# Kernel tuning notes

Hardware: AMD Instinct MI355X
Metric: run time of the kernel (lower is better)

Reference implementation:

```python
import jax, jax.numpy as jnp
import numpy as np

N_NODES = 200000
N_EDGES = 600000
NODE_IN = 32
EDGE_IN = 16
HID = 128
L = 3
MLP_HID = 128
LN_EPS = 1e-5


def _dense(k, fan_in, fan_out):
    kw, kb = jax.random.split(k)
    s = 1.0 / np.sqrt(fan_in)
    W = jax.random.uniform(kw, (fan_in, fan_out), jnp.float32, -s, s)
    b = jax.random.uniform(kb, (fan_out,), jnp.float32, -s, s)
    return W, b


def setup_inputs() -> dict:
    key = jax.random.key(0)
    ks = jax.random.split(key, 16)
    x = jax.random.normal(ks[0], (N_NODES, NODE_IN), jnp.float32)
    edge_index = jax.random.randint(ks[1], (2, N_EDGES), 0, N_NODES, jnp.int32)
    edge_attr = jax.random.normal(ks[2], (N_EDGES, EDGE_IN), jnp.float32)
    enc_w, enc_b = _dense(ks[3], NODE_IN, HID)
    ee_w, ee_b = _dense(ks[4], EDGE_IN, HID)
    w1s, b1s, w2s, b2s = [], [], [], []
    for i in range(L):
        W1, B1 = _dense(jax.random.fold_in(ks[5], i), HID, HID)
        W2, B2 = _dense(jax.random.fold_in(ks[6], i), HID, HID)
        w1s.append(W1); b1s.append(B1); w2s.append(W2); b2s.append(B2)
    gine_w1 = jnp.stack(w1s); gine_b1 = jnp.stack(b1s)
    gine_w2 = jnp.stack(w2s); gine_b2 = jnp.stack(b2s)
    gine_eps = jnp.zeros((L,), jnp.float32)  # PyG GINEConv default eps=0
    ln_g = jnp.ones((L, HID), jnp.float32)
    ln_b = jnp.zeros((L, HID), jnp.float32)
    mlp_w1, mlp_b1 = _dense(ks[7], 3 * HID, MLP_HID)
    mlp_w2, mlp_b2 = _dense(ks[8], MLP_HID, 1)
    return {"x": x, "edge_index": edge_index, "edge_attr": edge_attr,
            "enc_w": enc_w, "enc_b": enc_b, "ee_w": ee_w, "ee_b": ee_b,
            "gine_w1": gine_w1, "gine_b1": gine_b1, "gine_w2": gine_w2,
            "gine_b2": gine_b2, "gine_eps": gine_eps, "ln_g": ln_g, "ln_b": ln_b,
            "mlp_w1": mlp_w1, "mlp_b1": mlp_b1, "mlp_w2": mlp_w2, "mlp_b2": mlp_b2}


def reference(x, edge_index, edge_attr, enc_w, enc_b, ee_w, ee_b,
              gine_w1, gine_b1, gine_w2, gine_b2, gine_eps, ln_g, ln_b,
              mlp_w1, mlp_b1, mlp_w2, mlp_b2):
    src, dst = edge_index[0], edge_index[1]
    h = x @ enc_w + enc_b                      # [N, HID]
    e = edge_attr @ ee_w + ee_b                # [E, HID]
    for i in range(L):
        # GINEConv: out = MLP((1+eps)*x + sum_{j->i} relu(x_j + e_ji))
        msg = jax.nn.relu(h[src] + e)          # [E, HID] gather+fuse
        agg = jax.ops.segment_sum(msg, dst, num_segments=N_NODES)
        z = (1.0 + gine_eps[i]) * h + agg
        z = jax.nn.relu(z @ gine_w1[i] + gine_b1[i]) @ gine_w2[i] + gine_b2[i]
        # PyG LayerNorm (default mode='graph'): normalize over all nodes+features
        mu = jnp.mean(z)
        zc = z - mu
        var = jnp.mean(zc * zc)
        z = zc / jnp.sqrt(var + LN_EPS) * ln_g[i] + ln_b[i]
        h = jax.nn.relu(z)                     # dropout is identity at inference
    edge_inputs = jnp.concatenate([h[src], h[dst], e], axis=1)  # [E, 3*HID]
    hmid = jax.nn.relu(edge_inputs @ mlp_w1 + mlp_b1)
    logits = (hmid @ mlp_w2 + mlp_b2)[:, 0]    # [E]
    return logits
```

## Files before the change

### kernel.cpp

```cpp
#include <hip/hip_runtime.h>
#include <hip/hip_bf16.h>

#define N_NODES 200000
#define N_EDGES 600000
#define NODE_IN 32
#define EDGE_IN 16
#define HID     128
#define LN_EPS  1e-5f
#define SCAN_B  512
#define NBLK_SCAN 391

typedef __attribute__((ext_vector_type(8))) short short8;
typedef __attribute__((ext_vector_type(4))) float f32x4;

static __device__ __forceinline__ ushort f2b(float f) {
    unsigned u = __builtin_bit_cast(unsigned, f);
    unsigned r = (u + 0x7fffu + ((u >> 16) & 1u)) >> 16;
    return (ushort)r;
}
static __device__ __forceinline__ float b2f(ushort us) {
    unsigned u = ((unsigned)us) << 16;
    return __builtin_bit_cast(float, u);
}

__global__ __launch_bounds__(256) void k_csr_zero(int* __restrict__ deg)
{
    const int i = blockIdx.x * 256 + threadIdx.x;
    if (i < N_NODES) deg[i] = 0;
}

__global__ __launch_bounds__(256) void k_csr_deg(
    const int* __restrict__ ei, int* __restrict__ deg)
{
    const int e = blockIdx.x * 256 + threadIdx.x;
    if (e < N_EDGES) atomicAdd(&deg[ei[N_EDGES + e]], 1);
}

__global__ __launch_bounds__(SCAN_B) void k_scan1(
    const int* __restrict__ deg, int* __restrict__ part)
{
    __shared__ int s[SCAN_B];
    const int t = threadIdx.x, i = blockIdx.x * SCAN_B + t;
    s[t] = (i < N_NODES) ? deg[i] : 0;
    __syncthreads();
    for (int off = SCAN_B / 2; off; off >>= 1) {
        if (t < off) s[t] += s[t + off];
        __syncthreads();
    }
    if (t == 0) part[blockIdx.x] = s[0];
}

__global__ void k_scan2(int* __restrict__ part, int* __restrict__ rowptr)
{
    if (threadIdx.x == 0) {
        int run = 0;
        for (int b = 0; b < NBLK_SCAN; b++) { int x = part[b]; part[b] = run; run += x; }
        rowptr[N_NODES] = N_EDGES;
    }
}

__global__ __launch_bounds__(SCAN_B) void k_scan3(
    const int* __restrict__ deg, const int* __restrict__ part,
    int* __restrict__ rowptr, int* __restrict__ cursor)
{
    __shared__ int s[SCAN_B];
    const int t = threadIdx.x, i = blockIdx.x * SCAN_B + t;
    const int v = (i < N_NODES) ? deg[i] : 0;
    s[t] = v;
    __syncthreads();
    for (int off = 1; off < SCAN_B; off <<= 1) {
        int x = (t >= off) ? s[t - off] : 0;
        __syncthreads();
        s[t] += x;
        __syncthreads();
    }
    if (i < N_NODES) {
        const int ex = s[t] - v + part[blockIdx.x];
        rowptr[i] = ex;
        cursor[i] = ex;
    }
}

__global__ __launch_bounds__(256) void k_csr_fill(
    const int* __restrict__ ei, const float* __restrict__ ea,
    int* __restrict__ cursor, int* __restrict__ srcp,
    int* __restrict__ dstp, float* __restrict__ eap)
{
    const int e = blockIdx.x * 256 + threadIdx.x;
    if (e < N_EDGES) {
        const int d = ei[N_EDGES + e];
        const int slot = atomicAdd(&cursor[d], 1);
        srcp[slot] = ei[e];
        dstp[slot] = d;
        const float4* s4 = (const float4*)(ea + (size_t)e * EDGE_IN);
        float4* o4 = (float4*)(eap + (size_t)slot * EDGE_IN);
        o4[0] = s4[0]; o4[1] = s4[1]; o4[2] = s4[2]; o4[3] = s4[3];
    }
}

__global__ __launch_bounds__(256) void k_prep_g(
    const float* __restrict__ gw1, const float* __restrict__ gw2,
    ushort* __restrict__ wpk)
{
    const int gidx = blockIdx.x * 256 + threadIdx.x;
    const int m    = gidx >> 11;
    const int r    = gidx & 2047;
    const int lane = r & 63;
    const int ntkb = r >> 6;
    const int nt = ntkb & 7, kb = ntkb >> 3;
    const int n  = nt * 16 + (lane & 15);
    const int k0 = kb * 32 + (lane >> 4) * 8;
    const float* W = (m < 3) ? gw1 + (size_t)m * HID * HID
                             : gw2 + (size_t)(m - 3) * HID * HID;
    short8 v;
#pragma unroll
    for (int j = 0; j < 8; j++)
        v[j] = (short)f2b(W[(size_t)(k0 + j) * HID + n]);
    ((short8*)wpk)[gidx] = v;
}

__global__ __launch_bounds__(256) void k_prep_m(
    const float* __restrict__ mw1, ushort* __restrict__ w1p)
{
    const int gidx = blockIdx.x * 256 + threadIdx.x;
    const int lane = gidx & 63;
    const int ntkb = gidx >> 6;
    const int nt = ntkb & 7, kb = ntkb >> 3;
    const int n  = nt * 16 + (lane & 15);
    const int k0 = kb * 32 + (lane >> 4) * 8;
    short8 v;
#pragma unroll
    for (int j = 0; j < 8; j++)
        v[j] = (short)f2b(mw1[(size_t)(k0 + j) * HID + n]);
    ((short8*)w1p)[gidx] = v;
}

__global__ __launch_bounds__(256) void k_node_enc(
    const float* __restrict__ x, const float* __restrict__ w,
    const float* __restrict__ b, const float* __restrict__ epsp,
    ushort* __restrict__ hz, float* __restrict__ agg,
    float* __restrict__ red)
{
    __shared__ float sx[16][NODE_IN];
    const int tid = threadIdx.x;
    const int n0  = blockIdx.x * 16;
    float* sxf = &sx[0][0];
    sxf[tid]       = x[(size_t)n0 * NODE_IN + tid];
    sxf[tid + 256] = x[(size_t)n0 * NODE_IN + tid + 256];

    const int f   = tid & 127;
    const int grp = tid >> 7;
    float wcol[NODE_IN];
#pragma unroll
    for (int k = 0; k < NODE_IN; k++) wcol[k] = w[k * HID + f];
    const float bf = b[f];
    const float alpha = 1.0f + epsp[0];
    __syncthreads();

#pragma unroll
    for (int it = 0; it < 8; it++) {
        const int ln = it * 2 + grp;
        const int n  = n0 + ln;
        const float4* sx4 = (const float4*)sx[ln];
        float acc = bf;
#pragma unroll
        for (int k4 = 0; k4 < NODE_IN / 4; k4++) {
            float4 v = sx4[k4];
            acc += v.x * wcol[k4*4] + v.y * wcol[k4*4+1] +
                   v.z * wcol[k4*4+2] + v.w * wcol[k4*4+3];
        }
        hz[(size_t)n * HID + f]  = f2b(acc);
        agg[(size_t)n * HID + f] = alpha * acc;
    }
    if (blockIdx.x == 0 && tid == 0) { red[0] = 0.f; red[1] = 0.f; }
}

__global__ __launch_bounds__(256) void k_msg2(
    const ushort* __restrict__ hz, const int* __restrict__ srcp,
    const int* __restrict__ dstp, const float* __restrict__ eap,
    const float* __restrict__ eew, const float* __restrict__ eeb,
    float* __restrict__ agg)
{
    const int tid = threadIdx.x;
    const int f   = tid & 127;
    const int s0  = blockIdx.x * 16 + (tid >> 7) * 8;

    float wcol[EDGE_IN];
#pragma unroll
    for (int k = 0; k < EDGE_IN; k++) wcol[k] = eew[k * HID + f];
    const float bf = eeb[f];

    int   prev = dstp[s0];
    float sum  = 0.f;
#pragma unroll
    for (int it = 0; it < 8; it++) {
        const int s  = s0 + it;
        const int d  = dstp[s];
        const int sn = srcp[s];
        const float4* e4 = (const float4*)(eap + (size_t)s * EDGE_IN);
        float4 a0 = e4[0], a1 = e4[1], a2 = e4[2], a3 = e4[3];
        float ev = bf;
        ev += a0.x*wcol[0]  + a0.y*wcol[1]  + a0.z*wcol[2]  + a0.w*wcol[3];
        ev += a1.x*wcol[4]  + a1.y*wcol[5]  + a1.z*wcol[6]  + a1.w*wcol[7];
        ev += a2.x*wcol[8]  + a2.y*wcol[9]  + a2.z*wcol[10] + a2.w*wcol[11];
        ev += a3.x*wcol[12] + a3.y*wcol[13] + a3.z*wcol[14] + a3.w*wcol[15];
        const float m = fmaxf(b2f(hz[(size_t)sn * HID + f]) + ev, 0.f);
        if (d != prev) {
            atomicAdd(&agg[(size_t)prev * HID + f], sum);
            prev = d; sum = m;
        } else {
            sum += m;
        }
    }
    atomicAdd(&agg[(size_t)prev * HID + f], sum);
}

template<bool IN_BF16, bool RELU_OUT, bool REDUCE>
__global__ __launch_bounds__(256) void k_gemm(
    const void* in_, const short8* __restrict__ wp,
    const float* __restrict__ bias, ushort* out, float* __restrict__ red)
{
    __shared__ ushort sU[64][136];
    const int tid = threadIdx.x;
    const int m0  = blockIdx.x * 64;

    if constexpr (IN_BF16) {
        const short8* in8 = (const short8*)((const ushort*)in_ + (size_t)m0 * HID);
#pragma unroll
        for (int it = 0; it < 4; it++) {
            const int q = it * 256 + tid;
            const int r = q >> 4, c8 = q & 15;
            *(short8*)&sU[r][c8 * 8] = in8[q];
        }
    } else {
        const float4* in4 = (const float4*)((const float*)in_ + (size_t)m0 * HID);
#pragma unroll
        for (int it = 0; it < 8; it++) {
            const int q = it * 256 + tid;
            const int r = q >> 5, c4 = q & 31;
            float4 v = in4[q];
            ushort4 u;
            u.x = f2b(v.x); u.y = f2b(v.y); u.z = f2b(v.z); u.w = f2b(v.w);
            *(ushort4*)&sU[r][c4 * 4] = u;
        }
    }
    __syncthreads();

    const int lane = tid & 63;
    const int r0   = (tid >> 6) * 16;
    const int arow = r0 + (lane & 15);
    const int kg8  = (lane >> 4) * 8;
    f32x4 acc[8] = {};
    for (int kb = 0; kb < 4; kb++) {
        short8 af = *(const short8*)&sU[arow][kb * 32 + kg8];
#pragma unroll
        for (int nt = 0; nt < 8; nt++) {
            short8 bf8 = wp[(kb * 8 + nt) * 64 + lane];
            acc[nt] = __builtin_amdgcn_mfma_f32_16x16x32_bf16(af, bf8, acc[nt], 0, 0, 0);
        }
    }

    float lsum = 0.f, lsq = 0.f;
    const int rowb = m0 + r0 + (lane >> 4) * 4;
#pragma unroll
    for (int nt = 0; nt < 8; nt++) {
        const int c = nt * 16 + (lane & 15);
        const float bc = bias[c];
#pragma unroll
        for (int j = 0; j < 4; j++) {
            float o = acc[nt][j] + bc;
            if constexpr (RELU_OUT) o = fmaxf(o, 0.f);
            if constexpr (REDUCE) { lsum += o; lsq += o * o; }
            out[(size_t)(rowb + j) * HID + c] = f2b(o);
        }
    }

    if constexpr (REDUCE) {
#pragma unroll
        for (int off = 32; off; off >>= 1) {
            lsum += __shfl_down(lsum, off);
            lsq  += __shfl_down(lsq, off);
        }
        __shared__ float sws[4], swq[4];
        const int wid = tid >> 6;
        if ((tid & 63) == 0) { sws[wid] = lsum; swq[wid] = lsq; }
        __syncthreads();
        if (tid == 0) {
            atomicAdd(&red[0], sws[0] + sws[1] + sws[2] + sws[3]);
            atomicAdd(&red[1], swq[0] + swq[1] + swq[2] + swq[3]);
        }
    }
}

__global__ void k_lnfin(float* __restrict__ red)
{
    if (threadIdx.x == 0) {
        const float inv = 1.0f / ((float)N_NODES * (float)HID);
        const float mu  = red[0] * inv;
        const float var = red[1] * inv - mu * mu;
        red[2] = mu;
        red[3] = 1.0f / sqrtf(var + LN_EPS);
        red[0] = 0.f; red[1] = 0.f;
    }
}

template<bool FUSE_NEXT>
__global__ __launch_bounds__(256) void k_ln(
    ushort* hz, const float* __restrict__ red,
    const float* __restrict__ g, const float* __restrict__ b,
    const float* __restrict__ eps_next, float* __restrict__ agg)
{
    const float mu = red[2], rstd = red[3];
    const int i = blockIdx.x * 256 + threadIdx.x;
    short8 z8 = ((const short8*)hz)[i];
    const int cb = (i & 15) * 2;
    float4 g0 = ((const float4*)g)[cb],  g1 = ((const float4*)g)[cb + 1];
    float4 b0 = ((const float4*)b)[cb],  b1 = ((const float4*)b)[cb + 1];
    float o[8];
    o[0] = fmaxf((b2f((ushort)z8[0]) - mu) * rstd * g0.x + b0.x, 0.f);
    o[1] = fmaxf((b2f((ushort)z8[1]) - mu) * rstd * g0.y + b0.y, 0.f);
    o[2] = fmaxf((b2f((ushort)z8[2]) - mu) * rstd * g0.z + b0.z, 0.f);
    o[3] = fmaxf((b2f((ushort)z8[3]) - mu) * rstd * g0.w + b0.w, 0.f);
    o[4] = fmaxf((b2f((ushort)z8[4]) - mu) * rstd * g1.x + b1.x, 0.f);
    o[5] = fmaxf((b2f((ushort)z8[5]) - mu) * rstd * g1.y + b1.y, 0.f);
    o[6] = fmaxf((b2f((ushort)z8[6]) - mu) * rstd * g1.z + b1.z, 0.f);
    o[7] = fmaxf((b2f((ushort)z8[7]) - mu) * rstd * g1.w + b1.w, 0.f);
    short8 h8;
#pragma unroll
    for (int j = 0; j < 8; j++) h8[j] = (short)f2b(o[j]);
    ((short8*)hz)[i] = h8;
    if constexpr (FUSE_NEXT) {
        const float a = 1.0f + eps_next[0];
        float4 A0, A1;
        A0.x = a*o[0]; A0.y = a*o[1]; A0.z = a*o[2]; A0.w = a*o[3];
        A1.x = a*o[4]; A1.y = a*o[5]; A1.z = a*o[6]; A1.w = a*o[7];
        ((float4*)agg)[i * 2]     = A0;
        ((float4*)agg)[i * 2 + 1] = A1;
    }
}

__global__ __launch_bounds__(256) void k_mlp(
    const ushort* __restrict__ hz, const int* __restrict__ ei,
    const float* __restrict__ ea, const float* __restrict__ eew,
    const float* __restrict__ eeb,
    const ushort* __restrict__ w1p, const float* __restrict__ b1,
    const float* __restrict__ w2, const float* __restrict__ b2,
    float* __restrict__ out)
{
    __shared__ ushort sE[64][136];
    const int* __restrict__ src = ei;
    const int* __restrict__ dst = ei + N_EDGES;
    const int tid = threadIdx.x;
    const int e0  = blockIdx.x * 64;
    const int lane = tid & 63;
    const int wv   = tid >> 6;
    const int r0   = wv * 16;

    {
        const int f = tid & 127;
        float wcol[EDGE_IN];
#pragma unroll
        for (int k = 0; k < EDGE_IN; k++) wcol[k] = eew[k * HID + f];
        const float bf = eeb[f];
#pragma unroll
        for (int it = 0; it < 32; it++) {
            const int e = it * 2 + (tid >> 7);
            const float4* ea4 = (const float4*)(ea + (size_t)(e0 + e) * EDGE_IN);
            float ev = bf;
#pragma unroll
            for (int k4 = 0; k4 < EDGE_IN / 4; k4++) {
                float4 v = ea4[k4];
                ev += v.x * wcol[k4*4] + v.y * wcol[k4*4+1] +
                      v.z * wcol[k4*4+2] + v.w * wcol[k4*4+3];
            }
            sE[e][f] = f2b(ev);
        }
    }

    const int er = e0 + r0 + (lane & 15);
    const int kg = lane >> 4;
    const int ns = src[er], nd = dst[er];
    const short8* hb8 = (const short8*)hz;
    short8 af[8];
#pragma unroll
    for (int kb = 0; kb < 4; kb++) af[kb]     = hb8[(size_t)ns * 16 + kb * 4 + kg];
#pragma unroll
    for (int kb = 0; kb < 4; kb++) af[4 + kb] = hb8[(size_t)nd * 16 + kb * 4 + kg];
    __syncthreads();

    f32x4 acc[8] = {};
    const short8* bfr = (const short8*)w1p;
#pragma unroll
    for (int kb = 0; kb < 8; kb++) {
#pragma unroll
        for (int nt = 0; nt < 8; nt++) {
            short8 bfrag = bfr[(kb * 8 + nt) * 64 + lane];
            acc[nt] = __builtin_amdgcn_mfma_f32_16x16x32_bf16(af[kb], bfrag, acc[nt], 0, 0, 0);
        }
    }
#pragma unroll
    for (int kb = 8; kb < 12; kb++) {
        short8 ae = *(const short8*)&sE[r0 + (lane & 15)][(kb - 8) * 32 + kg * 8];
#pragma unroll
        for (int nt = 0; nt < 8; nt++) {
            short8 bfrag = bfr[(kb * 8 + nt) * 64 + lane];
            acc[nt] = __builtin_amdgcn_mfma_f32_16x16x32_bf16(ae, bfrag, acc[nt], 0, 0, 0);
        }
    }

    float s0 = 0.f, s1 = 0.f, s2 = 0.f, s3 = 0.f;
#pragma unroll
    for (int nt = 0; nt < 8; nt++) {
        const int col = nt * 16 + (lane & 15);
        const float b1c = b1[col];
        const float w2c = w2[col];
        s0 += fmaxf(acc[nt][0] + b1c, 0.f) * w2c;
        s1 += fmaxf(acc[nt][1] + b1c, 0.f) * w2c;
        s2 += fmaxf(acc[nt][2] + b1c, 0.f) * w2c;
        s3 += fmaxf(acc[nt][3] + b1c, 0.f) * w2c;
    }
#pragma unroll
    for (int m = 1; m < 16; m <<= 1) {
        s0 += __shfl_xor(s0, m); s1 += __shfl_xor(s1, m);
        s2 += __shfl_xor(s2, m); s3 += __shfl_xor(s3, m);
    }
    if ((lane & 15) == 0) {
        const float bb = b2[0];
        const int eb = e0 + r0 + kg * 4;
        out[eb + 0] = s0 + bb; out[eb + 1] = s1 + bb;
        out[eb + 2] = s2 + bb; out[eb + 3] = s3 + bb;
    }
}

extern "C" void kernel_launch(void* const* d_in, const int* in_sizes, int n_in,
                              void* d_out, int out_size, void* d_ws, size_t ws_size,
                              hipStream_t stream)
{
    const float* x    = (const float*)d_in[0];
    const int*   ei   = (const int*)  d_in[1];
    const float* ea   = (const float*)d_in[2];
    const float* encw = (const float*)d_in[3];
    const float* encb = (const float*)d_in[4];
    const float* eew  = (const float*)d_in[5];
    const float* eeb  = (const float*)d_in[6];
    const float* gw1  = (const float*)d_in[7];
    const float* gb1  = (const float*)d_in[8];
    const float* gw2  = (const float*)d_in[9];
    const float* gb2  = (const float*)d_in[10];
    const float* geps = (const float*)d_in[11];
    const float* lng  = (const float*)d_in[12];
    const float* lnb  = (const float*)d_in[13];
    const float* mw1  = (const float*)d_in[14];
    const float* mb1  = (const float*)d_in[15];
    const float* mw2  = (const float*)d_in[16];
    const float* mb2  = (const float*)d_in[17];

    float* ws = (float*)d_ws;
    const size_t NH = (size_t)N_NODES * HID;
    float*  agg  = ws;
    ushort* hz   = (ushort*)(ws + NH);
    float*  eap  = ws + NH + NH / 2;
    int*    srcp = (int*)(ws + 48000000);
    int*    dstp = (int*)(ws + 48600000);
    int*    deg  = (int*)(ws + 49200000);
    int*    rowp = (int*)(ws + 49400000);
    int*    curs = (int*)(ws + 49600064);
    int*    part = (int*)(ws + 49800064);
    float*  red  = ws + 49800640;
    ushort* wpk  = (ushort*)(ws + 49800704);
    ushort* w1p  = (ushort*)(ws + 49850000);

    k_prep_g<<<48, 256, 0, stream>>>(gw1, gw2, wpk);
    k_prep_m<<<24, 256, 0, stream>>>(mw1, w1p);
    k_csr_zero<<<(N_NODES + 255) / 256, 256, 0, stream>>>(deg);
    k_csr_deg<<<(N_EDGES + 255) / 256, 256, 0, stream>>>(ei, deg);
    k_scan1<<<NBLK_SCAN, SCAN_B, 0, stream>>>(deg, part);
    k_scan2<<<1, 64, 0, stream>>>(part, rowp);
    k_scan3<<<NBLK_SCAN, SCAN_B, 0, stream>>>(deg, part, rowp, curs);
    k_csr_fill<<<(N_EDGES + 255) / 256, 256, 0, stream>>>(ei, ea, curs,
                                                          srcp, dstp, eap);
    k_node_enc<<<N_NODES / 16, 256, 0, stream>>>(x, encw, encb, geps, hz, agg, red);

    const int LN_BLKS = (int)(NH / 8 / 256);
    for (int l = 0; l < 3; l++) {
        k_msg2<<<N_EDGES / 16, 256, 0, stream>>>(hz, srcp, dstp, eap,
                                                 eew, eeb, agg);
        k_gemm<false, true, false><<<N_NODES / 64, 256, 0, stream>>>(
            agg, (const short8*)wpk + (size_t)l * 2048,
            gb1 + (size_t)l * HID, hz, nullptr);
        k_gemm<true, false, true><<<N_NODES / 64, 256, 0, stream>>>(
            hz, (const short8*)wpk + (size_t)(3 + l) * 2048,
            gb2 + (size_t)l * HID, hz, red);
        k_lnfin<<<1, 64, 0, stream>>>(red);
        if (l < 2)
            k_ln<true><<<LN_BLKS, 256, 0, stream>>>(
                hz, red, lng + (size_t)l * HID, lnb + (size_t)l * HID,
                geps + l + 1, agg);
        else
            k_ln<false><<<LN_BLKS, 256, 0, stream>>>(
                hz, red, lng + (size_t)l * HID, lnb + (size_t)l * HID,
                nullptr, nullptr);
    }

    k_mlp<<<N_EDGES / 64, 256, 0, stream>>>(hz, ei, ea, eew, eeb,
                                            w1p, mb1, mw2, mb2, (float*)d_out);
}
```

Before: 1.571 ms.

## Fuse GIN MLP GEMMs and run edge MLP in dst-sorted order

The two per-layer GEMMs are merged into one kernel that keeps the ReLU intermediate in shared memory as bf16. This avoids writing the hidden activation to global memory and reading it back, and saves a launch per layer. The final edge MLP now walks edges in the CSR (dst-sorted) order, using the permuted edge attributes and a new edge-id array to scatter the outputs back to their original positions. The sorted order is meant to improve locality of the destination-node gathers, at the cost of an extra index array and scattered output writes.

```diff
diff --git a/kernel.cpp b/kernel.cpp
--- a/kernel.cpp
+++ b/kernel.cpp
@@ -84,7 +84,7 @@
 __global__ __launch_bounds__(256) void k_csr_fill(
     const int* __restrict__ ei, const float* __restrict__ ea,
     int* __restrict__ cursor, int* __restrict__ srcp,
-    int* __restrict__ dstp, float* __restrict__ eap)
+    int* __restrict__ dstp, int* __restrict__ eidp, float* __restrict__ eap)
 {
     const int e = blockIdx.x * 256 + threadIdx.x;
     if (e < N_EDGES) {
@@ -92,6 +92,7 @@
         const int slot = atomicAdd(&cursor[d], 1);
         srcp[slot] = ei[e];
         dstp[slot] = d;
+        eidp[slot] = e;
         const float4* s4 = (const float4*)(ea + (size_t)e * EDGE_IN);
         float4* o4 = (float4*)(eap + (size_t)slot * EDGE_IN);
         o4[0] = s4[0]; o4[1] = s4[1]; o4[2] = s4[2]; o4[3] = s4[3];
@@ -215,34 +216,25 @@
     atomicAdd(&agg[(size_t)prev * HID + f], sum);
 }
 
-template<bool IN_BF16, bool RELU_OUT, bool REDUCE>
-__global__ __launch_bounds__(256) void k_gemm(
-    const void* in_, const short8* __restrict__ wp,
-    const float* __restrict__ bias, ushort* out, float* __restrict__ red)
+__global__ __launch_bounds__(256) void k_gemm12(
+    const float* __restrict__ in_, const short8* __restrict__ wp1,
+    const float* __restrict__ bias1, const short8* __restrict__ wp2,
+    const float* __restrict__ bias2, ushort* __restrict__ out,
+    float* __restrict__ red)
 {
     __shared__ ushort sU[64][136];
     const int tid = threadIdx.x;
     const int m0  = blockIdx.x * 64;
 
-    if constexpr (IN_BF16) {
-        const short8* in8 = (const short8*)((const ushort*)in_ + (size_t)m0 * HID);
-#pragma unroll
-        for (int it = 0; it < 4; it++) {
-            const int q = it * 256 + tid;
-            const int r = q >> 4, c8 = q & 15;
-            *(short8*)&sU[r][c8 * 8] = in8[q];
-        }
-    } else {
-        const float4* in4 = (const float4*)((const float*)in_ + (size_t)m0 * HID);
-#pragma unroll
-        for (int it = 0; it < 8; it++) {
-            const int q = it * 256 + tid;
-            const int r = q >> 5, c4 = q & 31;
-            float4 v = in4[q];
-            ushort4 u;
-            u.x = f2b(v.x); u.y = f2b(v.y); u.z = f2b(v.z); u.w = f2b(v.w);
-            *(ushort4*)&sU[r][c4 * 4] = u;
-        }
+    const float4* in4 = (const float4*)(in_ + (size_t)m0 * HID);
+#pragma unroll
+    for (int it = 0; it < 8; it++) {
+        const int q = it * 256 + tid;
+        const int r = q >> 5, c4 = q & 31;
+        float4 v = in4[q];
+        ushort4 u;
+        u.x = f2b(v.x); u.y = f2b(v.y); u.z = f2b(v.z); u.w = f2b(v.w);
+        *(ushort4*)&sU[r][c4 * 4] = u;
     }
     __syncthreads();
 
@@ -250,45 +242,64 @@
     const int r0   = (tid >> 6) * 16;
     const int arow = r0 + (lane & 15);
     const int kg8  = (lane >> 4) * 8;
+
     f32x4 acc[8] = {};
     for (int kb = 0; kb < 4; kb++) {
         short8 af = *(const short8*)&sU[arow][kb * 32 + kg8];
 #pragma unroll
         for (int nt = 0; nt < 8; nt++) {
-            short8 bf8 = wp[(kb * 8 + nt) * 64 + lane];
+            short8 bf8 = wp1[(kb * 8 + nt) * 64 + lane];
             acc[nt] = __builtin_amdgcn_mfma_f32_16x16x32_bf16(af, bf8, acc[nt], 0, 0, 0);
         }
     }
-
-    float lsum = 0.f, lsq = 0.f;
-    const int rowb = m0 + r0 + (lane >> 4) * 4;
+    __syncthreads();
+
+    const int rloc = r0 + (lane >> 4) * 4;
 #pragma unroll
     for (int nt = 0; nt < 8; nt++) {
         const int c = nt * 16 + (lane & 15);
-        const float bc = bias[c];
+        const float bc = bias1[c];
+#pragma unroll
+        for (int j = 0; j < 4; j++)
+            sU[rloc + j][c] = f2b(fmaxf(acc[nt][j] + bc, 0.f));
+    }
+    __syncthreads();
+
+    f32x4 acc2[8] = {};
+    for (int kb = 0; kb < 4; kb++) {
+        short8 af = *(const short8*)&sU[arow][kb * 32 + kg8];
+#pragma unroll
+        for (int nt = 0; nt < 8; nt++) {
+            short8 bf8 = wp2[(kb * 8 + nt) * 64 + lane];
+            acc2[nt] = __builtin_amdgcn_mfma_f32_16x16x32_bf16(af, bf8, acc2[nt], 0, 0, 0);
+        }
+    }
+
+    float lsum = 0.f, lsq = 0.f;
+    const int rowb = m0 + rloc;
+#pragma unroll
+    for (int nt = 0; nt < 8; nt++) {
+        const int c = nt * 16 + (lane & 15);
+        const float bc = bias2[c];
 #pragma unroll
         for (int j = 0; j < 4; j++) {
-            float o = acc[nt][j] + bc;
-            if constexpr (RELU_OUT) o = fmaxf(o, 0.f);
-            if constexpr (REDUCE) { lsum += o; lsq += o * o; }
+            float o = acc2[nt][j] + bc;
+            lsum += o; lsq += o * o;
             out[(size_t)(rowb + j) * HID + c] = f2b(o);
         }
     }
-
-    if constexpr (REDUCE) {
-#pragma unroll
-        for (int off = 32; off; off >>= 1) {
-            lsum += __shfl_down(lsum, off);
-            lsq  += __shfl_down(lsq, off);
-        }
-        __shared__ float sws[4], swq[4];
-        const int wid = tid >> 6;
-        if ((tid & 63) == 0) { sws[wid] = lsum; swq[wid] = lsq; }
-        __syncthreads();
-        if (tid == 0) {
-            atomicAdd(&red[0], sws[0] + sws[1] + sws[2] + sws[3]);
-            atomicAdd(&red[1], swq[0] + swq[1] + swq[2] + swq[3]);
-        }
+#pragma unroll
+    for (int off = 32; off; off >>= 1) {
+        lsum += __shfl_down(lsum, off);
+        lsq  += __shfl_down(lsq, off);
+    }
+    __shared__ float sws[4], swq[4];
+    const int wid = tid >> 6;
+    if ((tid & 63) == 0) { sws[wid] = lsum; swq[wid] = lsq; }
+    __syncthreads();
+    if (tid == 0) {
+        atomicAdd(&red[0], sws[0] + sws[1] + sws[2] + sws[3]);
+        atomicAdd(&red[1], swq[0] + swq[1] + swq[2] + swq[3]);
     }
 }
 
@@ -340,16 +351,15 @@
 }
 
 __global__ __launch_bounds__(256) void k_mlp(
-    const ushort* __restrict__ hz, const int* __restrict__ ei,
-    const float* __restrict__ ea, const float* __restrict__ eew,
+    const ushort* __restrict__ hz, const int* __restrict__ srcp,
+    const int* __restrict__ dstp, const int* __restrict__ eidp,
+    const float* __restrict__ eap, const float* __restrict__ eew,
     const float* __restrict__ eeb,
     const ushort* __restrict__ w1p, const float* __restrict__ b1,
     const float* __restrict__ w2, const float* __restrict__ b2,
     float* __restrict__ out)
 {
     __shared__ ushort sE[64][136];
-    const int* __restrict__ src = ei;
-    const int* __restrict__ dst = ei + N_EDGES;
     const int tid = threadIdx.x;
     const int e0  = blockIdx.x * 64;
     const int lane = tid & 63;
@@ -365,7 +375,7 @@
 #pragma unroll
         for (int it = 0; it < 32; it++) {
             const int e = it * 2 + (tid >> 7);
-            const float4* ea4 = (const float4*)(ea + (size_t)(e0 + e) * EDGE_IN);
+            const float4* ea4 = (const float4*)(eap + (size_t)(e0 + e) * EDGE_IN);
             float ev = bf;
 #pragma unroll
             for (int k4 = 0; k4 < EDGE_IN / 4; k4++) {
@@ -377,9 +387,9 @@
         }
     }
 
-    const int er = e0 + r0 + (lane & 15);
-    const int kg = lane >> 4;
-    const int ns = src[er], nd = dst[er];
+    const int slot = e0 + r0 + (lane & 15);
+    const int kg   = lane >> 4;
+    const int ns = srcp[slot], nd = dstp[slot];
     const short8* hb8 = (const short8*)hz;
     short8 af[8];
 #pragma unroll
@@ -426,9 +436,9 @@
     }
     if ((lane & 15) == 0) {
         const float bb = b2[0];
-        const int eb = e0 + r0 + kg * 4;
-        out[eb + 0] = s0 + bb; out[eb + 1] = s1 + bb;
-        out[eb + 2] = s2 + bb; out[eb + 3] = s3 + bb;
+        const int sb = e0 + r0 + kg * 4;
+        out[eidp[sb + 0]] = s0 + bb; out[eidp[sb + 1]] = s1 + bb;
+        out[eidp[sb + 2]] = s2 + bb; out[eidp[sb + 3]] = s3 + bb;
     }
 }
 
@@ -462,13 +472,14 @@
     float*  eap  = ws + NH + NH / 2;
     int*    srcp = (int*)(ws + 48000000);
     int*    dstp = (int*)(ws + 48600000);
-    int*    deg  = (int*)(ws + 49200000);
-    int*    rowp = (int*)(ws + 49400000);
-    int*    curs = (int*)(ws + 49600064);
-    int*    part = (int*)(ws + 49800064);
-    float*  red  = ws + 49800640;
-    ushort* wpk  = (ushort*)(ws + 49800704);
-    ushort* w1p  = (ushort*)(ws + 49850000);
+    int*    eidp = (int*)(ws + 49200000);
+    int*    deg  = (int*)(ws + 49800000);
+    int*    rowp = (int*)(ws + 50000000);
+    int*    curs = (int*)(ws + 50200064);
+    int*    part = (int*)(ws + 50400064);
+    float*  red  = ws + 50400640;
+    ushort* wpk  = (ushort*)(ws + 50400704);
+    ushort* w1p  = (ushort*)(ws + 50449856);
 
     k_prep_g<<<48, 256, 0, stream>>>(gw1, gw2, wpk);
     k_prep_m<<<24, 256, 0, stream>>>(mw1, w1p);
@@ -478,19 +489,17 @@
     k_scan2<<<1, 64, 0, stream>>>(part, rowp);
     k_scan3<<<NBLK_SCAN, SCAN_B, 0, stream>>>(deg, part, rowp, curs);
     k_csr_fill<<<(N_EDGES + 255) / 256, 256, 0, stream>>>(ei, ea, curs,
-                                                          srcp, dstp, eap);
+                                                          srcp, dstp, eidp, eap);
     k_node_enc<<<N_NODES / 16, 256, 0, stream>>>(x, encw, encb, geps, hz, agg, red);
 
     const int LN_BLKS = (int)(NH / 8 / 256);
     for (int l = 0; l < 3; l++) {
         k_msg2<<<N_EDGES / 16, 256, 0, stream>>>(hz, srcp, dstp, eap,
                                                  eew, eeb, agg);
-        k_gemm<false, true, false><<<N_NODES / 64, 256, 0, stream>>>(
-            agg, (const short8*)wpk + (size_t)l * 2048,
-            gb1 + (size_t)l * HID, hz, nullptr);
-        k_gemm<true, false, true><<<N_NODES / 64, 256, 0, stream>>>(
-            hz, (const short8*)wpk + (size_t)(3 + l) * 2048,
-            gb2 + (size_t)l * HID, hz, red);
+        k_gemm12<<<N_NODES / 64, 256, 0, stream>>>(
+            agg, (const short8*)wpk + (size_t)l * 2048, gb1 + (size_t)l * HID,
+            (const short8*)wpk + (size_t)(3 + l) * 2048, gb2 + (size_t)l * HID,
+            hz, red);
         k_lnfin<<<1, 64, 0, stream>>>(red);
         if (l < 2)
             k_ln<true><<<LN_BLKS, 256, 0, stream>>>(
@@ -502,6 +511,7 @@
                 nullptr, nullptr);
     }
 
-    k_mlp<<<N_EDGES / 64, 256, 0, stream>>>(hz, ei, ea, eew, eeb,
-                                            w1p, mb1, mw2, mb2, (float*)d_out);
-}
+    k_mlp<<<N_EDGES / 64, 256, 0, stream>>>(hz, srcp, dstp, eidp, eap,
+                                            eew, eeb, w1p, mb1, mw2, mb2,
+                                            (float*)d_out);
+}
```

After: 1.478 ms. -5.9%, faster.
